# Kernel tuning notes

Measured on AMD Instinct MI355X. Metric: run time of the kernel, lower is better.

Reference implementation:

```python
import jax, jax.numpy as jnp
import numpy as np

N, E, D_IN, D_OUT = 50000, 300000, 256, 256
BN_EPS = 1e-5


def ccorr(a, b):
    # circular correlation: irfft(conj(rfft(a)) * rfft(b))
    return jnp.fft.irfft(jnp.conj(jnp.fft.rfft(a, axis=-1)) * jnp.fft.rfft(b, axis=-1), n=a.shape[-1], axis=-1)


def setup_inputs() -> dict:
    key = jax.random.key(0)
    ks = jax.random.split(key, 8)
    return {
        "node_ft": jax.random.normal(ks[0], (N, D_IN), dtype=jnp.float32),
        "edge_ft": jax.random.normal(ks[1], (E, D_IN), dtype=jnp.float32),
        "norm": jax.random.uniform(ks[2], (N, 1), dtype=jnp.float32),
        "w_loop": jax.random.normal(ks[3], (D_IN, D_OUT), dtype=jnp.float32) * (1.414 / np.sqrt(D_IN)),
        "w_in": jax.random.normal(ks[4], (D_IN, D_OUT), dtype=jnp.float32) * (1.414 / np.sqrt(D_IN)),
        "loop_rel": jax.random.normal(ks[5], (1, D_IN), dtype=jnp.float32),
        "w_bias": jnp.zeros((D_OUT,), dtype=jnp.float32),
        "bn_gamma": jnp.ones((D_OUT,), dtype=jnp.float32),
        "bn_beta": jnp.zeros((D_OUT,), dtype=jnp.float32),
        "src": jax.random.randint(ks[6], (E,), 0, N, dtype=jnp.int32),
        "dst": jax.random.randint(ks[7], (E,), 0, N, dtype=jnp.int32),
    }


def reference(node_ft, edge_ft, norm, w_loop, w_in, loop_rel, w_bias, bn_gamma, bn_beta, src, dst):
    n_nodes = node_ft.shape[0]
    # self-loop message: ccorr(ft, loop_rel) @ w_loop  [N, d_out]
    loop_msg = ccorr(node_ft, loop_rel) @ w_loop
    # per-edge message: ccorr(src_ft, edge_ft) @ w_in  [E, d_out]
    msg = ccorr(node_ft[src], edge_ft) @ w_in
    # scatter-sum aggregation then norm multiply (apply_func)
    agg = jax.ops.segment_sum(msg, dst, num_segments=n_nodes) * norm
    h = agg + w_bias + loop_msg
    # BatchNorm1d (training mode: batch stats, biased variance)
    mean = jnp.mean(h, axis=0)
    var = jnp.var(h, axis=0)
    h = (h - mean) * jax.lax.rsqrt(var + BN_EPS) * bn_gamma + bn_beta
    return jnp.tanh(h)
```

## Files before the change

kernel.cpp:

```cpp
#include <hip/hip_runtime.h>
#include <hip/hip_bf16.h>

#define NN 50000
#define BN_EPS 1e-5f
#define NFW 288
#define TWOPI_256 0.024543692606170259f

typedef __attribute__((ext_vector_type(8))) _Float16 half8;
typedef __attribute__((ext_vector_type(2))) _Float16 half2v;
typedef __attribute__((ext_vector_type(4))) float f32x4;
#define MFMA16F __builtin_amdgcn_mfma_f32_16x16x32_f16

__device__ __align__(16) _Float16 g_NF[(size_t)NN * NFW];
__device__ float g_LOOPM[(size_t)NN * 256];
__device__ float g_Wle[256 * 256];
__device__ __align__(16) unsigned short g_FB[8 * 20 * 64 * 8];
__device__ __align__(16) unsigned short g_CB[9 * 16 * 64 * 8];
__device__ __align__(16) unsigned short g_WLEB[8 * 16 * 64 * 8];

__device__ __forceinline__ void atomAddF(float* p, float v) { unsafeAtomicAdd(p, v); }

__device__ __forceinline__ unsigned short f2hu(float x) {
    union { _Float16 f; unsigned short u; } c;
    c.f = (_Float16)x;
    return c.u;
}

__device__ __forceinline__ void stage_h64(const float* __restrict__ base,
                                          long long row0, long long maxrow,
                                          unsigned short* A, int t) {
#pragma unroll
    for (int q = 0; q < 8; ++q) {
        int idx = q * 512 + t;
        int row = idx >> 6, c4 = idx & 63;
        long long gr = row0 + row;
        if (gr >= maxrow) gr = maxrow - 1;
        float4 v = ((const float4*)base)[gr * 64 + c4];
        union { _Float16 f[4]; ushort4 u; } r;
        r.f[0] = (_Float16)v.x; r.f[1] = (_Float16)v.y;
        r.f[2] = (_Float16)v.z; r.f[3] = (_Float16)v.w;
        int ks = c4 >> 3;
        int off = ((row >> 4) * 8 + ks) * 1024 +
                  ((((((c4 >> 1) & 3) << 4) | (row & 15)) * 16) ^ (ks << 4)) +
                  (c4 & 1) * 8;
        *(ushort4*)((char*)A + off) = r.u;
    }
}

__global__ __launch_bounds__(256) void wle_kernel(
    const float* __restrict__ loop_rel, const float* __restrict__ w_loop,
    float* __restrict__ W_le) {
    __shared__ float lr[256];
    const int d = threadIdx.x, j = blockIdx.x;
    lr[d] = loop_rel[d];
    __syncthreads();
    float acc = 0.f;
#pragma unroll 4
    for (int k = 0; k < 256; ++k)
        acc = fmaf(lr[(j + k) & 255], w_loop[k * 256 + d], acc);
    W_le[j * 256 + d] = acc;
}

__global__ __launch_bounds__(512) void fb_pack() {
    int b = blockIdx.x, ks = b / 20, nt = b % 20;
    int t = threadIdx.x, lane = t >> 3, e = t & 7;
    int k = 32 * ks + 8 * (lane >> 4) + e;
    int r2 = nt * 16 + (lane & 15);
    float val = 0.f;
    if (r2 < 258) {
        int f = r2 >> 1;
        int m = (f * k) & 255;
        float s, c;
        sincosf((float)m * TWOPI_256, &s, &c);
        val = (r2 & 1) ? -s : c;
    }
    g_FB[((ks * 20 + nt) * 64 + lane) * 8 + e] = f2hu(val);
}

__global__ __launch_bounds__(512) void cb_pack(const float* __restrict__ w_in) {
    __shared__ float ct[256], st[256];
    int t = threadIdx.x;
    if (t < 256) {
        float s, c;
        sincosf((float)t * TWOPI_256, &s, &c);
        ct[t] = c; st[t] = s;
    }
    __syncthreads();
    int b = blockIdx.x, ks = b / 16, nt = b % 16;
    int lane = t >> 3, e = t & 7;
    int kk = 32 * ks + 8 * (lane >> 4) + e;
    int d = nt * 16 + (lane & 15);
    float val = 0.f;
    if (kk < 258) {
        int f = kk >> 1;
        float cf = (f == 0 || f == 128) ? (1.f / 256.f) : (2.f / 256.f);
        const float* tab = (kk & 1) ? st : ct;
        float sgn = (kk & 1) ? -1.f : 1.f;
        float acc = 0.f;
        for (int k = 0; k < 256; ++k)
            acc = fmaf(tab[(f * k) & 255], w_in[k * 256 + d], acc);
        val = cf * sgn * acc;
    }
    g_CB[((ks * 16 + nt) * 64 + lane) * 8 + e] = f2hu(val);
}

__global__ __launch_bounds__(512) void wleb_pack() {
    int b = blockIdx.x, ks = b / 16, nt = b % 16;
    int t = threadIdx.x, lane = t >> 3, e = t & 7;
    int k = 32 * ks + 8 * (lane >> 4) + e;
    int d = nt * 16 + (lane & 15);
    g_WLEB[((ks * 16 + nt) * 64 + lane) * 8 + e] = f2hu(g_Wle[k * 256 + d]);
}

__global__ __launch_bounds__(512, 4) void nfloop_kernel(
    const float* __restrict__ node_ft, int N) {
    __shared__ char smem[32768];
    unsigned short* A = (unsigned short*)smem;
    const int t = threadIdx.x;
    const long long r0 = (long long)blockIdx.x * 64;
    stage_h64(node_ft, r0, N, A, t);
    __syncthreads();

    const int lane = t & 63, w = t >> 6;
    const int mw = w >> 2, nw = w & 3;
    const int l15 = lane & 15, lg = lane >> 4;

    {
        f32x4 acc[2][5] = {};
#pragma unroll
        for (int ks = 0; ks < 8; ++ks) {
            half8 a0 = *(const half8*)((char*)A + ((2 * mw + 0) * 8 + ks) * 1024 + ((lane * 16) ^ (ks << 4)));
            half8 a1 = *(const half8*)((char*)A + ((2 * mw + 1) * 8 + ks) * 1024 + ((lane * 16) ^ (ks << 4)));
#pragma unroll
            for (int j = 0; j < 4; ++j) {
                int tn = nw + 4 * j;
                half8 bf = *(const half8*)(g_FB + ((size_t)(ks * 20 + tn) * 64 + lane) * 8);
                acc[0][j] = MFMA16F(a0, bf, acc[0][j], 0, 0, 0);
                acc[1][j] = MFMA16F(a1, bf, acc[1][j], 0, 0, 0);
            }
            if (nw == 0) {
                half8 bf = *(const half8*)(g_FB + ((size_t)(ks * 20 + 16) * 64 + lane) * 8);
                acc[0][4] = MFMA16F(a0, bf, acc[0][4], 0, 0, 0);
                acc[1][4] = MFMA16F(a1, bf, acc[1][4], 0, 0, 0);
            }
        }
#pragma unroll
        for (int mt = 0; mt < 2; ++mt)
#pragma unroll
            for (int j = 0; j < 5; ++j) {
                int tn = nw + 4 * j;
                if (tn > 16 || (j == 4 && nw != 0)) continue;
                int r2 = tn * 16 + l15;
#pragma unroll
                for (int r = 0; r < 4; ++r) {
                    long long gr = r0 + (2 * mw + mt) * 16 + lg * 4 + r;
                    if (gr < N && r2 < 258)
                        g_NF[gr * NFW + r2] = (_Float16)acc[mt][j][r];
                }
            }
    }
    {
        f32x4 acc[2][4] = {};
#pragma unroll
        for (int ks = 0; ks < 8; ++ks) {
            half8 a0 = *(const half8*)((char*)A + ((2 * mw + 0) * 8 + ks) * 1024 + ((lane * 16) ^ (ks << 4)));
            half8 a1 = *(const half8*)((char*)A + ((2 * mw + 1) * 8 + ks) * 1024 + ((lane * 16) ^ (ks << 4)));
#pragma unroll
            for (int j = 0; j < 4; ++j) {
                half8 bf = *(const half8*)(g_WLEB + ((size_t)(ks * 16 + 4 * nw + j) * 64 + lane) * 8);
                acc[0][j] = MFMA16F(a0, bf, acc[0][j], 0, 0, 0);
                acc[1][j] = MFMA16F(a1, bf, acc[1][j], 0, 0, 0);
            }
        }
#pragma unroll
        for (int mt = 0; mt < 2; ++mt)
#pragma unroll
            for (int j = 0; j < 4; ++j)
#pragma unroll
                for (int r = 0; r < 4; ++r) {
                    long long gr = r0 + (2 * mw + mt) * 16 + lg * 4 + r;
                    if (gr < N)
                        g_LOOPM[gr * 256 + (4 * nw + j) * 16 + l15] = acc[mt][j][r];
                }
    }
}

__global__ __launch_bounds__(512, 4) void edge_kernel(
    const float* __restrict__ edge_ft, const int* __restrict__ src,
    const int* __restrict__ dst, float* __restrict__ agg, int E) {
    __shared__ char smem[36864 + 512];
    unsigned short* A = (unsigned short*)smem;
    unsigned short* Z = (unsigned short*)smem;
    int* sdd = (int*)(smem + 36864);

    const int t = threadIdx.x;
    const long long ebase = (long long)blockIdx.x * 64;
    const int lane = t & 63, w = t >> 6;
    const int mw = w >> 2, nw = w & 3;
    const int l15 = lane & 15, lg = lane >> 4;
    const bool odd = (l15 & 1);

    int srcv[2][4];
#pragma unroll
    for (int mt = 0; mt < 2; ++mt)
#pragma unroll
        for (int r = 0; r < 4; ++r) {
            long long ge = ebase + (2 * mw + mt) * 16 + lg * 4 + r;
            srcv[mt][r] = src[ge < E ? ge : 0];
        }

    if (t < 64) {
        long long ge = ebase + t;
        sdd[t] = dst[ge < E ? ge : 0];
    }
    stage_h64(edge_ft, ebase, E, A, t);

    unsigned int pf[2][5][4];
#pragma unroll
    for (int mt = 0; mt < 2; ++mt)
#pragma unroll
        for (int j = 0; j < 5; ++j) {
            int tn = nw + 4 * j;
            if (tn >= 17) continue;
            int r2 = tn * 16 + l15;
            if (r2 < 258) {
#pragma unroll
                for (int r = 0; r < 4; ++r)
                    pf[mt][j][r] = *(const unsigned int*)(g_NF +
                        (long long)srcv[mt][r] * NFW + (r2 & ~1));
            }
        }
    __syncthreads();

    f32x4 acc1[2][5] = {};
#pragma unroll
    for (int ks = 0; ks < 8; ++ks) {
        half8 a0 = *(const half8*)((char*)A + ((2 * mw + 0) * 8 + ks) * 1024 + ((lane * 16) ^ (ks << 4)));
        half8 a1 = *(const half8*)((char*)A + ((2 * mw + 1) * 8 + ks) * 1024 + ((lane * 16) ^ (ks << 4)));
#pragma unroll
        for (int j = 0; j < 4; ++j) {
            int tn = nw + 4 * j;
            half8 bf = *(const half8*)(g_FB + ((size_t)(ks * 20 + tn) * 64 + lane) * 8);
            acc1[0][j] = MFMA16F(a0, bf, acc1[0][j], 0, 0, 0);
            acc1[1][j] = MFMA16F(a1, bf, acc1[1][j], 0, 0, 0);
        }
        if (nw == 0) {
            half8 bf = *(const half8*)(g_FB + ((size_t)(ks * 20 + 16) * 64 + lane) * 8);
            acc1[0][4] = MFMA16F(a0, bf, acc1[0][4], 0, 0, 0);
            acc1[1][4] = MFMA16F(a1, bf, acc1[1][4], 0, 0, 0);
        }
    }
    __syncthreads();

#pragma unroll
    for (int mt = 0; mt < 2; ++mt) {
        int tm = 2 * mw + mt;
#pragma unroll
        for (int j = 0; j < 5; ++j) {
            int tn = nw + 4 * j;
            if (tn >= 18) continue;
            int r2 = tn * 16 + l15;
#pragma unroll
            for (int r = 0; r < 4; ++r) {
                int e = tm * 16 + lg * 4 + r;
                float z = 0.f;
                if (r2 < 258) {
                    float own = acc1[mt][j][r];
                    float oth = __shfl_xor(own, 1);
                    union { unsigned int u; half2v h; } cv;
                    cv.u = pf[mt][j][r];
                    float br = (float)cv.h[0], bi = (float)cv.h[1];
                    z = odd ? (br * own - bi * oth) : (br * own + bi * oth);
                }
                int ksz = r2 >> 5;
                int off = ((e >> 4) * 9 + ksz) * 1024 +
                          ((((((r2 >> 3) & 3) << 4) | (e & 15)) * 16) ^ (ksz << 4)) +
                          (r2 & 7) * 2;
                *(unsigned short*)((char*)Z + off) = f2hu(z);
            }
        }
    }
    __syncthreads();

    f32x4 acc2[2][4] = {};
#pragma unroll
    for (int ks = 0; ks < 9; ++ks) {
        half8 a0 = *(const half8*)((char*)Z + ((2 * mw + 0) * 9 + ks) * 1024 + ((lane * 16) ^ (ks << 4)));
        half8 a1 = *(const half8*)((char*)Z + ((2 * mw + 1) * 9 + ks) * 1024 + ((lane * 16) ^ (ks << 4)));
#pragma unroll
        for (int j = 0; j < 4; ++j) {
            half8 bf = *(const half8*)(g_CB + ((size_t)(ks * 16 + 4 * nw + j) * 64 + lane) * 8);
            acc2[0][j] = MFMA16F(a0, bf, acc2[0][j], 0, 0, 0);
            acc2[1][j] = MFMA16F(a1, bf, acc2[1][j], 0, 0, 0);
        }
    }

#pragma unroll
    for (int mt = 0; mt < 2; ++mt)
#pragma unroll
        for (int j = 0; j < 4; ++j)
#pragma unroll
            for (int r = 0; r < 4; ++r) {
                int e = (2 * mw + mt) * 16 + lg * 4 + r;
                if (ebase + e < E) {
                    int dr = sdd[e];
                    int d = (4 * nw + j) * 16 + l15;
                    atomAddF(agg + (long long)dr * 256 + d, acc2[mt][j][r]);
                }
            }
}

__global__ __launch_bounds__(256) void combine_kernel(
    const float* __restrict__ norm, const float* __restrict__ w_bias,
    float* __restrict__ hbuf, float* __restrict__ s1g, float* __restrict__ s2g,
    int N) {
    __shared__ float s1l[256], s2l[256];
    const int tid = threadIdx.x;
    s1l[tid] = 0.f;
    s2l[tid] = 0.f;
    __syncthreads();
    const int r0 = blockIdx.x * 32;
    const int dg = tid & 63, rg = tid >> 6;
    const float4 bv = ((const float4*)w_bias)[dg];
    float4* h4 = (float4*)hbuf;
    const float4* lp4 = (const float4*)g_LOOPM;
    float s1[4] = {0.f, 0.f, 0.f, 0.f}, s2[4] = {0.f, 0.f, 0.f, 0.f};
#pragma unroll
    for (int r8 = 0; r8 < 8; ++r8) {
        int r = r0 + rg * 8 + r8;
        if (r < N) {
            float nrm = norm[r];
            float4 av = h4[(long long)r * 64 + dg];
            float4 lv = lp4[(long long)r * 64 + dg];
            float h0 = fmaf(av.x, nrm, bv.x + lv.x);
            float h1 = fmaf(av.y, nrm, bv.y + lv.y);
            float h2 = fmaf(av.z, nrm, bv.z + lv.z);
            float h3 = fmaf(av.w, nrm, bv.w + lv.w);
            h4[(long long)r * 64 + dg] = make_float4(h0, h1, h2, h3);
            s1[0] += h0; s2[0] += h0 * h0;
            s1[1] += h1; s2[1] += h1 * h1;
            s1[2] += h2; s2[2] += h2 * h2;
            s1[3] += h3; s2[3] += h3 * h3;
        }
    }
#pragma unroll
    for (int c = 0; c < 4; ++c) {
        atomicAdd(&s1l[dg * 4 + c], s1[c]);
        atomicAdd(&s2l[dg * 4 + c], s2[c]);
    }
    __syncthreads();
    atomAddF(&s1g[tid], s1l[tid]);
    atomAddF(&s2g[tid], s2l[tid]);
}

__global__ __launch_bounds__(256) void finalize_kernel(
    float* __restrict__ out, const float* __restrict__ s1g,
    const float* __restrict__ s2g, const float* __restrict__ gamma,
    const float* __restrict__ beta, int N) {
    long long i4 = (long long)blockIdx.x * blockDim.x + threadIdx.x;
    long long tot = (long long)N * 64;
    if (i4 >= tot) return;
    const int dg = (int)(i4 & 63);
    float4 h = ((float4*)out)[i4];
    const float4 s1 = ((const float4*)s1g)[dg];
    const float4 s2 = ((const float4*)s2g)[dg];
    const float4 g = ((const float4*)gamma)[dg];
    const float4 b = ((const float4*)beta)[dg];
    const float invN = 1.f / (float)N;
    float4 o;
    { float m = s1.x * invN; float v = s2.x * invN - m * m;
      o.x = tanhf(fmaf(h.x - m, rsqrtf(v + BN_EPS) * g.x, b.x)); }
    { float m = s1.y * invN; float v = s2.y * invN - m * m;
      o.y = tanhf(fmaf(h.y - m, rsqrtf(v + BN_EPS) * g.y, b.y)); }
    { float m = s1.z * invN; float v = s2.z * invN - m * m;
      o.z = tanhf(fmaf(h.z - m, rsqrtf(v + BN_EPS) * g.z, b.z)); }
    { float m = s1.w * invN; float v = s2.w * invN - m * m;
      o.w = tanhf(fmaf(h.w - m, rsqrtf(v + BN_EPS) * g.w, b.w)); }
    ((float4*)out)[i4] = o;
}

extern "C" void kernel_launch(void* const* d_in, const int* in_sizes, int n_in,
                              void* d_out, int out_size, void* d_ws, size_t ws_size,
                              hipStream_t stream) {
    const float* node_ft  = (const float*)d_in[0];
    const float* edge_ft  = (const float*)d_in[1];
    const float* norm     = (const float*)d_in[2];
    const float* w_loop   = (const float*)d_in[3];
    const float* w_in     = (const float*)d_in[4];
    const float* loop_rel = (const float*)d_in[5];
    const float* w_bias   = (const float*)d_in[6];
    const float* bn_gamma = (const float*)d_in[7];
    const float* bn_beta  = (const float*)d_in[8];
    const int*   src      = (const int*)d_in[9];
    const int*   dst      = (const int*)d_in[10];

    const int N = in_sizes[2];
    const int E = in_sizes[9];
    float* out = (float*)d_out;

    float* s1g = (float*)d_ws;
    float* s2g = s1g + 256;

    hipMemsetAsync(d_out, 0, (size_t)N * 256 * sizeof(float), stream);
    hipMemsetAsync(d_ws, 0, 512 * sizeof(float), stream);

    float* Wle_ptr = nullptr;
    hipGetSymbolAddress((void**)&Wle_ptr, HIP_SYMBOL(g_Wle));

    wle_kernel<<<256, 256, 0, stream>>>(loop_rel, w_loop, Wle_ptr);
    fb_pack<<<8 * 20, 512, 0, stream>>>();
    cb_pack<<<9 * 16, 512, 0, stream>>>(w_in);
    wleb_pack<<<8 * 16, 512, 0, stream>>>();
    nfloop_kernel<<<(N + 63) / 64, 512, 0, stream>>>(node_ft, N);
    edge_kernel<<<(E + 63) / 64, 512, 0, stream>>>(edge_ft, src, dst, out, E);
    combine_kernel<<<(N + 31) / 32, 256, 0, stream>>>(norm, w_bias, out, s1g, s2g, N);
    finalize_kernel<<<(int)(((long long)N * 64 + 255) / 256), 256, 0, stream>>>(
        out, s1g, s2g, bn_gamma, bn_beta, N);
}
```

Measured before the change: 526.0 us.

## Make edge kernel persistent with double-buffered LDS prefetch of next tile

The edge kernel becomes persistent, with a grid capped at 512 blocks that each loop over 64-edge tiles in strides. While one tile is being computed, the block loads the next tile's edge features, src/dst indices and gathered node spectra into registers, then writes them into a second LDS buffer, so global load latency overlaps with MFMA work. It also swaps __syncthreads for raw s_waitcnt+s_barrier. The cost is twice the LDS per block (about 74KB), which can lower occupancy, plus more live registers from the staging arrays.

```diff
diff --git a/kernel.cpp b/kernel.cpp
--- a/kernel.cpp
+++ b/kernel.cpp
@@ -10,6 +10,8 @@
 typedef __attribute__((ext_vector_type(2))) _Float16 half2v;
 typedef __attribute__((ext_vector_type(4))) float f32x4;
 #define MFMA16F __builtin_amdgcn_mfma_f32_16x16x32_f16
+
+#define BARRIER_LDS() asm volatile("s_waitcnt lgkmcnt(0)\ns_barrier" ::: "memory")
 
 __device__ __align__(16) _Float16 g_NF[(size_t)NN * NFW];
 __device__ float g_LOOPM[(size_t)NN * 256];
@@ -26,24 +28,19 @@
     return c.u;
 }
 
-__device__ __forceinline__ void stage_h64(const float* __restrict__ base,
-                                          long long row0, long long maxrow,
-                                          unsigned short* A, int t) {
+__device__ __forceinline__ void stage_write(char* A, const float4* stg, int t) {
 #pragma unroll
     for (int q = 0; q < 8; ++q) {
         int idx = q * 512 + t;
         int row = idx >> 6, c4 = idx & 63;
-        long long gr = row0 + row;
-        if (gr >= maxrow) gr = maxrow - 1;
-        float4 v = ((const float4*)base)[gr * 64 + c4];
         union { _Float16 f[4]; ushort4 u; } r;
-        r.f[0] = (_Float16)v.x; r.f[1] = (_Float16)v.y;
-        r.f[2] = (_Float16)v.z; r.f[3] = (_Float16)v.w;
+        r.f[0] = (_Float16)stg[q].x; r.f[1] = (_Float16)stg[q].y;
+        r.f[2] = (_Float16)stg[q].z; r.f[3] = (_Float16)stg[q].w;
         int ks = c4 >> 3;
         int off = ((row >> 4) * 8 + ks) * 1024 +
                   ((((((c4 >> 1) & 3) << 4) | (row & 15)) * 16) ^ (ks << 4)) +
                   (c4 & 1) * 8;
-        *(ushort4*)((char*)A + off) = r.u;
+        *(ushort4*)(A + off) = r.u;
     }
 }
 
@@ -118,7 +115,17 @@
     unsigned short* A = (unsigned short*)smem;
     const int t = threadIdx.x;
     const long long r0 = (long long)blockIdx.x * 64;
-    stage_h64(node_ft, r0, N, A, t);
+    {
+        float4 stg[8];
+#pragma unroll
+        for (int q = 0; q < 8; ++q) {
+            int idx = q * 512 + t;
+            long long gr = r0 + (idx >> 6);
+            if (gr >= N) gr = N - 1;
+            stg[q] = ((const float4*)node_ft)[gr * 64 + (idx & 63)];
+        }
+        stage_write(smem, stg, t);
+    }
     __syncthreads();
 
     const int lane = t & 63, w = t >> 6;
@@ -187,127 +194,196 @@
 
 __global__ __launch_bounds__(512, 4) void edge_kernel(
     const float* __restrict__ edge_ft, const int* __restrict__ src,
-    const int* __restrict__ dst, float* __restrict__ agg, int E) {
-    __shared__ char smem[36864 + 512];
-    unsigned short* A = (unsigned short*)smem;
-    unsigned short* Z = (unsigned short*)smem;
-    int* sdd = (int*)(smem + 36864);
+    const int* __restrict__ dst, float* __restrict__ agg, int E, int ntiles) {
+    __shared__ char smem[2 * 36864 + 512];
+    int* sdd = (int*)(smem + 2 * 36864);
 
     const int t = threadIdx.x;
-    const long long ebase = (long long)blockIdx.x * 64;
     const int lane = t & 63, w = t >> 6;
     const int mw = w >> 2, nw = w & 3;
     const int l15 = lane & 15, lg = lane >> 4;
     const bool odd = (l15 & 1);
-
-    int srcv[2][4];
-#pragma unroll
-    for (int mt = 0; mt < 2; ++mt)
-#pragma unroll
-        for (int r = 0; r < 4; ++r) {
-            long long ge = ebase + (2 * mw + mt) * 16 + lg * 4 + r;
-            srcv[mt][r] = src[ge < E ? ge : 0];
-        }
-
-    if (t < 64) {
-        long long ge = ebase + t;
-        sdd[t] = dst[ge < E ? ge : 0];
-    }
-    stage_h64(edge_ft, ebase, E, A, t);
-
+    const int G = gridDim.x;
+
+    long long T = blockIdx.x;
     unsigned int pf[2][5][4];
-#pragma unroll
-    for (int mt = 0; mt < 2; ++mt)
-#pragma unroll
-        for (int j = 0; j < 5; ++j) {
-            int tn = nw + 4 * j;
-            if (tn >= 17) continue;
-            int r2 = tn * 16 + l15;
-            if (r2 < 258) {
-#pragma unroll
-                for (int r = 0; r < 4; ++r)
-                    pf[mt][j][r] = *(const unsigned int*)(g_NF +
-                        (long long)srcv[mt][r] * NFW + (r2 & ~1));
-            }
-        }
-    __syncthreads();
-
-    f32x4 acc1[2][5] = {};
-#pragma unroll
-    for (int ks = 0; ks < 8; ++ks) {
-        half8 a0 = *(const half8*)((char*)A + ((2 * mw + 0) * 8 + ks) * 1024 + ((lane * 16) ^ (ks << 4)));
-        half8 a1 = *(const half8*)((char*)A + ((2 * mw + 1) * 8 + ks) * 1024 + ((lane * 16) ^ (ks << 4)));
-#pragma unroll
-        for (int j = 0; j < 4; ++j) {
-            int tn = nw + 4 * j;
-            half8 bf = *(const half8*)(g_FB + ((size_t)(ks * 20 + tn) * 64 + lane) * 8);
-            acc1[0][j] = MFMA16F(a0, bf, acc1[0][j], 0, 0, 0);
-            acc1[1][j] = MFMA16F(a1, bf, acc1[1][j], 0, 0, 0);
-        }
-        if (nw == 0) {
-            half8 bf = *(const half8*)(g_FB + ((size_t)(ks * 20 + 16) * 64 + lane) * 8);
-            acc1[0][4] = MFMA16F(a0, bf, acc1[0][4], 0, 0, 0);
-            acc1[1][4] = MFMA16F(a1, bf, acc1[1][4], 0, 0, 0);
-        }
-    }
-    __syncthreads();
-
-#pragma unroll
-    for (int mt = 0; mt < 2; ++mt) {
-        int tm = 2 * mw + mt;
-#pragma unroll
-        for (int j = 0; j < 5; ++j) {
-            int tn = nw + 4 * j;
-            if (tn >= 18) continue;
-            int r2 = tn * 16 + l15;
+
+    {
+        long long ebase = T * 64;
+        int srcv[2][4];
+#pragma unroll
+        for (int mt = 0; mt < 2; ++mt)
 #pragma unroll
             for (int r = 0; r < 4; ++r) {
-                int e = tm * 16 + lg * 4 + r;
-                float z = 0.f;
+                long long ge = ebase + (2 * mw + mt) * 16 + lg * 4 + r;
+                srcv[mt][r] = src[ge < E ? ge : 0];
+            }
+        float4 stg[8];
+#pragma unroll
+        for (int q = 0; q < 8; ++q) {
+            int idx = q * 512 + t;
+            long long gr = ebase + (idx >> 6);
+            if (gr >= E) gr = E - 1;
+            stg[q] = ((const float4*)edge_ft)[gr * 64 + (idx & 63)];
+        }
+        if (t < 64) {
+            long long ge = ebase + t;
+            sdd[t] = dst[ge < E ? ge : 0];
+        }
+#pragma unroll
+        for (int mt = 0; mt < 2; ++mt)
+#pragma unroll
+            for (int j = 0; j < 5; ++j) {
+                int tn = nw + 4 * j;
+                if (tn >= 17) continue;
+                int r2 = tn * 16 + l15;
                 if (r2 < 258) {
-                    float own = acc1[mt][j][r];
-                    float oth = __shfl_xor(own, 1);
-                    union { unsigned int u; half2v h; } cv;
-                    cv.u = pf[mt][j][r];
-                    float br = (float)cv.h[0], bi = (float)cv.h[1];
-                    z = odd ? (br * own - bi * oth) : (br * own + bi * oth);
-                }
-                int ksz = r2 >> 5;
-                int off = ((e >> 4) * 9 + ksz) * 1024 +
-                          ((((((r2 >> 3) & 3) << 4) | (e & 15)) * 16) ^ (ksz << 4)) +
-                          (r2 & 7) * 2;
-                *(unsigned short*)((char*)Z + off) = f2hu(z);
-            }
-        }
-    }
-    __syncthreads();
-
-    f32x4 acc2[2][4] = {};
-#pragma unroll
-    for (int ks = 0; ks < 9; ++ks) {
-        half8 a0 = *(const half8*)((char*)Z + ((2 * mw + 0) * 9 + ks) * 1024 + ((lane * 16) ^ (ks << 4)));
-        half8 a1 = *(const half8*)((char*)Z + ((2 * mw + 1) * 9 + ks) * 1024 + ((lane * 16) ^ (ks << 4)));
-#pragma unroll
-        for (int j = 0; j < 4; ++j) {
-            half8 bf = *(const half8*)(g_CB + ((size_t)(ks * 16 + 4 * nw + j) * 64 + lane) * 8);
-            acc2[0][j] = MFMA16F(a0, bf, acc2[0][j], 0, 0, 0);
-            acc2[1][j] = MFMA16F(a1, bf, acc2[1][j], 0, 0, 0);
-        }
-    }
-
-#pragma unroll
-    for (int mt = 0; mt < 2; ++mt)
-#pragma unroll
-        for (int j = 0; j < 4; ++j)
-#pragma unroll
-            for (int r = 0; r < 4; ++r) {
-                int e = (2 * mw + mt) * 16 + lg * 4 + r;
-                if (ebase + e < E) {
-                    int dr = sdd[e];
-                    int d = (4 * nw + j) * 16 + l15;
-                    atomAddF(agg + (long long)dr * 256 + d, acc2[mt][j][r]);
-                }
-            }
+#pragma unroll
+                    for (int r = 0; r < 4; ++r)
+                        pf[mt][j][r] = *(const unsigned int*)(g_NF +
+                            (long long)srcv[mt][r] * NFW + (r2 & ~1));
+                }
+            }
+        stage_write(smem, stg, t);
+    }
+    BARRIER_LDS();
+
+    int c = 0;
+    while (true) {
+        char* AB = smem + c * 36864;
+        const long long ebase = T * 64;
+        const long long Tn = T + G;
+        const bool has_next = (Tn < ntiles);
+
+        f32x4 acc1[2][5] = {};
+#pragma unroll
+        for (int ks = 0; ks < 8; ++ks) {
+            half8 a0 = *(const half8*)(AB + ((0 * 8 + ks)) * 1024 + ((lane * 16) ^ (ks << 4)) + mw * 16384);
+            half8 a1 = *(const half8*)(AB + ((1 * 8 + ks)) * 1024 + ((lane * 16) ^ (ks << 4)) + mw * 16384);
+#pragma unroll
+            for (int j = 0; j < 4; ++j) {
+                int tn = nw + 4 * j;
+                half8 bf = *(const half8*)(g_FB + ((size_t)(ks * 20 + tn) * 64 + lane) * 8);
+                acc1[0][j] = MFMA16F(a0, bf, acc1[0][j], 0, 0, 0);
+                acc1[1][j] = MFMA16F(a1, bf, acc1[1][j], 0, 0, 0);
+            }
+            if (nw == 0) {
+                half8 bf = *(const half8*)(g_FB + ((size_t)(ks * 20 + 16) * 64 + lane) * 8);
+                acc1[0][4] = MFMA16F(a0, bf, acc1[0][4], 0, 0, 0);
+                acc1[1][4] = MFMA16F(a1, bf, acc1[1][4], 0, 0, 0);
+            }
+        }
+        BARRIER_LDS();
+
+#pragma unroll
+        for (int mt = 0; mt < 2; ++mt) {
+            int tm = 2 * mw + mt;
+#pragma unroll
+            for (int j = 0; j < 5; ++j) {
+                int tn = nw + 4 * j;
+                if (tn >= 18) continue;
+                int r2 = tn * 16 + l15;
+#pragma unroll
+                for (int r = 0; r < 4; ++r) {
+                    int e = tm * 16 + lg * 4 + r;
+                    float z = 0.f;
+                    if (r2 < 258) {
+                        float own = acc1[mt][j][r];
+                        float oth = __shfl_xor(own, 1);
+                        union { unsigned int u; half2v h; } cv;
+                        cv.u = pf[mt][j][r];
+                        float br = (float)cv.h[0], bi = (float)cv.h[1];
+                        z = odd ? (br * own - bi * oth) : (br * own + bi * oth);
+                    }
+                    int ksz = r2 >> 5;
+                    int off = ((e >> 4) * 9 + ksz) * 1024 +
+                              ((((((r2 >> 3) & 3) << 4) | (e & 15)) * 16) ^ (ksz << 4)) +
+                              (r2 & 7) * 2;
+                    *(unsigned short*)(AB + off) = f2hu(z);
+                }
+            }
+        }
+
+        int nsrc[2][4];
+        float4 nstg[8];
+        int ndst = 0;
+        if (has_next) {
+            long long nb = Tn * 64;
+#pragma unroll
+            for (int mt = 0; mt < 2; ++mt)
+#pragma unroll
+                for (int r = 0; r < 4; ++r) {
+                    long long ge = nb + (2 * mw + mt) * 16 + lg * 4 + r;
+                    nsrc[mt][r] = src[ge < E ? ge : 0];
+                }
+#pragma unroll
+            for (int q = 0; q < 8; ++q) {
+                int idx = q * 512 + t;
+                long long gr = nb + (idx >> 6);
+                if (gr >= E) gr = E - 1;
+                nstg[q] = ((const float4*)edge_ft)[gr * 64 + (idx & 63)];
+            }
+            if (t < 64) {
+                long long ge = nb + t;
+                ndst = dst[ge < E ? ge : 0];
+            }
+        }
+        BARRIER_LDS();
+
+        f32x4 acc2[2][4] = {};
+#pragma unroll
+        for (int ks = 0; ks < 9; ++ks) {
+            half8 a0 = *(const half8*)(AB + ((0 * 9 + ks)) * 1024 + ((lane * 16) ^ (ks << 4)) + mw * 18432);
+            half8 a1 = *(const half8*)(AB + ((1 * 9 + ks)) * 1024 + ((lane * 16) ^ (ks << 4)) + mw * 18432);
+#pragma unroll
+            for (int j = 0; j < 4; ++j) {
+                half8 bf = *(const half8*)(g_CB + ((size_t)(ks * 16 + 4 * nw + j) * 64 + lane) * 8);
+                acc2[0][j] = MFMA16F(a0, bf, acc2[0][j], 0, 0, 0);
+                acc2[1][j] = MFMA16F(a1, bf, acc2[1][j], 0, 0, 0);
+            }
+        }
+
+        if (has_next) {
+#pragma unroll
+            for (int mt = 0; mt < 2; ++mt)
+#pragma unroll
+                for (int j = 0; j < 5; ++j) {
+                    int tn = nw + 4 * j;
+                    if (tn >= 17) continue;
+                    int r2 = tn * 16 + l15;
+                    if (r2 < 258) {
+#pragma unroll
+                        for (int r = 0; r < 4; ++r)
+                            pf[mt][j][r] = *(const unsigned int*)(g_NF +
+                                (long long)nsrc[mt][r] * NFW + (r2 & ~1));
+                    }
+                }
+        }
+
+        if (has_next) {
+            stage_write(smem + (c ^ 1) * 36864, nstg, t);
+            if (t < 64) sdd[(c ^ 1) * 64 + t] = ndst;
+        }
+
+#pragma unroll
+        for (int mt = 0; mt < 2; ++mt)
+#pragma unroll
+            for (int j = 0; j < 4; ++j)
+#pragma unroll
+                for (int r = 0; r < 4; ++r) {
+                    int e = (2 * mw + mt) * 16 + lg * 4 + r;
+                    if (ebase + e < E) {
+                        int dr = sdd[c * 64 + e];
+                        atomAddF(agg + (long long)dr * 256 + (4 * nw + j) * 16 + l15,
+                                 acc2[mt][j][r]);
+                    }
+                }
+
+        if (!has_next) break;
+        BARRIER_LDS();
+        c ^= 1;
+        T = Tn;
+    }
 }
 
 __global__ __launch_bounds__(256) void combine_kernel(
@@ -407,12 +483,15 @@
     float* Wle_ptr = nullptr;
     hipGetSymbolAddress((void**)&Wle_ptr, HIP_SYMBOL(g_Wle));
 
+    const int ntiles = (E + 63) / 64;
+    const int egrid = ntiles < 512 ? ntiles : 512;
+
     wle_kernel<<<256, 256, 0, stream>>>(loop_rel, w_loop, Wle_ptr);
     fb_pack<<<8 * 20, 512, 0, stream>>>();
     cb_pack<<<9 * 16, 512, 0, stream>>>(w_in);
     wleb_pack<<<8 * 16, 512, 0, stream>>>();
     nfloop_kernel<<<(N + 63) / 64, 512, 0, stream>>>(node_ft, N);
-    edge_kernel<<<(E + 63) / 64, 512, 0, stream>>>(edge_ft, src, dst, out, E);
+    edge_kernel<<<egrid, 512, 0, stream>>>(edge_ft, src, dst, out, E, ntiles);
     combine_kernel<<<(N + 31) / 32, 256, 0, stream>>>(norm, w_bias, out, s1g, s2g, N);
     finalize_kernel<<<(int)(((long long)N * 64 + 255) / 256), 256, 0, stream>>>(
         out, s1g, s2g, bn_gamma, bn_beta, N);
```

After: 1.321 ms. +151.2%, slower.

## Sort edges by destination and fuse loop message, bias and norm into outputs

Applied to the files above, without the earlier changes.

Adds a counting sort of edges by destination (histogram, three-pass scan, permutation) so each edge block handles edges grouped by destination node. The edge kernel then pre-sums runs of equal destinations within a lane before issuing fewer atomics. The loop message and bias are written straight into the output, and norm is applied per edge. This removes the separate loop-message buffer, the output memset and the combine pass, replacing them with a read-only stats pass. In exchange it adds several small sort kernels and gathers edge_ft rows indirectly through the permutation, which makes those loads less coalesced.

```diff
diff --git a/kernel.cpp b/kernel.cpp
--- a/kernel.cpp
+++ b/kernel.cpp
@@ -2,6 +2,7 @@
 #include <hip/hip_bf16.h>
 
 #define NN 50000
+#define EE 300000
 #define BN_EPS 1e-5f
 #define NFW 288
 #define TWOPI_256 0.024543692606170259f
@@ -12,11 +13,16 @@
 #define MFMA16F __builtin_amdgcn_mfma_f32_16x16x32_f16
 
 __device__ __align__(16) _Float16 g_NF[(size_t)NN * NFW];
-__device__ float g_LOOPM[(size_t)NN * 256];
 __device__ float g_Wle[256 * 256];
 __device__ __align__(16) unsigned short g_FB[8 * 20 * 64 * 8];
 __device__ __align__(16) unsigned short g_CB[9 * 16 * 64 * 8];
 __device__ __align__(16) unsigned short g_WLEB[8 * 16 * 64 * 8];
+__device__ int g_hist[NN];
+__device__ int g_off[NN];
+__device__ int g_cursor[NN];
+__device__ int g_perm[EE];
+__device__ int g_bsum[128];
+__device__ int g_bbase[128];
 
 __device__ __forceinline__ void atomAddF(float* p, float v) { unsafeAtomicAdd(p, v); }
 
@@ -26,24 +32,74 @@
     return c.u;
 }
 
-__device__ __forceinline__ void stage_h64(const float* __restrict__ base,
-                                          long long row0, long long maxrow,
-                                          unsigned short* A, int t) {
+__device__ __forceinline__ void stage_write(char* A, const float4* stg, int t) {
 #pragma unroll
     for (int q = 0; q < 8; ++q) {
         int idx = q * 512 + t;
         int row = idx >> 6, c4 = idx & 63;
-        long long gr = row0 + row;
-        if (gr >= maxrow) gr = maxrow - 1;
-        float4 v = ((const float4*)base)[gr * 64 + c4];
         union { _Float16 f[4]; ushort4 u; } r;
-        r.f[0] = (_Float16)v.x; r.f[1] = (_Float16)v.y;
-        r.f[2] = (_Float16)v.z; r.f[3] = (_Float16)v.w;
+        r.f[0] = (_Float16)stg[q].x; r.f[1] = (_Float16)stg[q].y;
+        r.f[2] = (_Float16)stg[q].z; r.f[3] = (_Float16)stg[q].w;
         int ks = c4 >> 3;
         int off = ((row >> 4) * 8 + ks) * 1024 +
                   ((((((c4 >> 1) & 3) << 4) | (row & 15)) * 16) ^ (ks << 4)) +
                   (c4 & 1) * 8;
-        *(ushort4*)((char*)A + off) = r.u;
+        *(ushort4*)(A + off) = r.u;
+    }
+}
+
+__global__ __launch_bounds__(512) void hist_kernel(const int* __restrict__ dst, int E) {
+    int e = blockIdx.x * 512 + threadIdx.x;
+    if (e < E) atomicAdd(&g_hist[dst[e]], 1);
+}
+
+__global__ __launch_bounds__(512) void scanA_kernel(int N) {
+    __shared__ int arr[512];
+    int t = threadIdx.x, b = blockIdx.x * 512 + t;
+    int cnt = (b < N) ? g_hist[b] : 0;
+    arr[t] = cnt;
+    __syncthreads();
+#pragma unroll
+    for (int off = 1; off < 512; off <<= 1) {
+        int v = (t >= off) ? arr[t - off] : 0;
+        __syncthreads();
+        arr[t] += v;
+        __syncthreads();
+    }
+    if (b < N) g_off[b] = arr[t] - cnt;
+    if (t == 511) g_bsum[blockIdx.x] = arr[511];
+}
+
+__global__ __launch_bounds__(128) void scanB_kernel(int nblk) {
+    __shared__ int arr[128];
+    int t = threadIdx.x;
+    int v0 = (t < nblk) ? g_bsum[t] : 0;
+    arr[t] = v0;
+    __syncthreads();
+#pragma unroll
+    for (int off = 1; off < 128; off <<= 1) {
+        int v = (t >= off) ? arr[t - off] : 0;
+        __syncthreads();
+        arr[t] += v;
+        __syncthreads();
+    }
+    if (t < nblk) g_bbase[t] = arr[t] - v0;
+}
+
+__global__ __launch_bounds__(512) void scanC_kernel(int N) {
+    int b = blockIdx.x * 512 + threadIdx.x;
+    if (b < N) {
+        int v = g_off[b] + g_bbase[blockIdx.x];
+        g_off[b] = v;
+        g_cursor[b] = v;
+    }
+}
+
+__global__ __launch_bounds__(512) void perm_kernel(const int* __restrict__ dst, int E) {
+    int e = blockIdx.x * 512 + threadIdx.x;
+    if (e < E) {
+        int pos = atomicAdd(&g_cursor[dst[e]], 1);
+        g_perm[pos] = e;
     }
 }
 
@@ -113,12 +169,23 @@
 }
 
 __global__ __launch_bounds__(512, 4) void nfloop_kernel(
-    const float* __restrict__ node_ft, int N) {
+    const float* __restrict__ node_ft, const float* __restrict__ w_bias,
+    float* __restrict__ out, int N) {
     __shared__ char smem[32768];
     unsigned short* A = (unsigned short*)smem;
     const int t = threadIdx.x;
     const long long r0 = (long long)blockIdx.x * 64;
-    stage_h64(node_ft, r0, N, A, t);
+    {
+        float4 stg[8];
+#pragma unroll
+        for (int q = 0; q < 8; ++q) {
+            int idx = q * 512 + t;
+            long long gr = r0 + (idx >> 6);
+            if (gr >= N) gr = N - 1;
+            stg[q] = ((const float4*)node_ft)[gr * 64 + (idx & 63)];
+        }
+        stage_write(smem, stg, t);
+    }
     __syncthreads();
 
     const int lane = t & 63, w = t >> 6;
@@ -173,25 +240,30 @@
             }
         }
 #pragma unroll
-        for (int mt = 0; mt < 2; ++mt)
-#pragma unroll
-            for (int j = 0; j < 4; ++j)
+        for (int j = 0; j < 4; ++j) {
+            const int col = (4 * nw + j) * 16 + l15;
+            const float bj = w_bias[col];
+#pragma unroll
+            for (int mt = 0; mt < 2; ++mt)
 #pragma unroll
                 for (int r = 0; r < 4; ++r) {
                     long long gr = r0 + (2 * mw + mt) * 16 + lg * 4 + r;
                     if (gr < N)
-                        g_LOOPM[gr * 256 + (4 * nw + j) * 16 + l15] = acc[mt][j][r];
+                        out[gr * 256 + col] = acc[mt][j][r] + bj;
                 }
+        }
     }
 }
 
 __global__ __launch_bounds__(512, 4) void edge_kernel(
-    const float* __restrict__ edge_ft, const int* __restrict__ src,
-    const int* __restrict__ dst, float* __restrict__ agg, int E) {
+    const float* __restrict__ edge_ft, const float* __restrict__ norm,
+    const int* __restrict__ src, const int* __restrict__ dst,
+    float* __restrict__ agg, int E) {
     __shared__ char smem[36864 + 512];
     unsigned short* A = (unsigned short*)smem;
     unsigned short* Z = (unsigned short*)smem;
     int* sdd = (int*)(smem + 36864);
+    float* snrm = (float*)(smem + 36864 + 256);
 
     const int t = threadIdx.x;
     const long long ebase = (long long)blockIdx.x * 64;
@@ -206,14 +278,25 @@
 #pragma unroll
         for (int r = 0; r < 4; ++r) {
             long long ge = ebase + (2 * mw + mt) * 16 + lg * 4 + r;
-            srcv[mt][r] = src[ge < E ? ge : 0];
+            if (ge >= E) ge = E - 1;
+            srcv[mt][r] = src[g_perm[ge]];
         }
 
     if (t < 64) {
         long long ge = ebase + t;
-        sdd[t] = dst[ge < E ? ge : 0];
-    }
-    stage_h64(edge_ft, ebase, E, A, t);
+        if (ge >= E) ge = E - 1;
+        int d = dst[g_perm[ge]];
+        sdd[t] = d;
+        snrm[t] = norm[d];
+    }
+
+    float4 stg[8];
+#pragma unroll
+    for (int q = 0; q < 8; ++q) {
+        long long ge = ebase + q * 8 + (t >> 6);
+        if (ge >= E) ge = E - 1;
+        stg[q] = ((const float4*)edge_ft)[(long long)g_perm[ge] * 64 + (t & 63)];
+    }
 
     unsigned int pf[2][5][4];
 #pragma unroll
@@ -230,6 +313,7 @@
                         (long long)srcv[mt][r] * NFW + (r2 & ~1));
             }
         }
+    stage_write(smem, stg, t);
     __syncthreads();
 
     f32x4 acc1[2][5] = {};
@@ -296,61 +380,64 @@
     }
 
 #pragma unroll
-    for (int mt = 0; mt < 2; ++mt)
-#pragma unroll
-        for (int j = 0; j < 4; ++j)
-#pragma unroll
-            for (int r = 0; r < 4; ++r) {
-                int e = (2 * mw + mt) * 16 + lg * 4 + r;
-                if (ebase + e < E) {
-                    int dr = sdd[e];
-                    int d = (4 * nw + j) * 16 + l15;
-                    atomAddF(agg + (long long)dr * 256 + d, acc2[mt][j][r]);
+    for (int mt = 0; mt < 2; ++mt) {
+        const int e0 = (2 * mw + mt) * 16 + lg * 4;
+        const bool v0 = ebase + e0 < E, v1 = ebase + e0 + 1 < E;
+        const bool v2 = ebase + e0 + 2 < E, v3 = ebase + e0 + 3 < E;
+        const int d0 = sdd[e0], d1 = sdd[e0 + 1], d2 = sdd[e0 + 2], d3 = sdd[e0 + 3];
+        const float n0 = snrm[e0], n1 = snrm[e0 + 1], n2 = snrm[e0 + 2], n3 = snrm[e0 + 3];
+        const bool uni = v3 && (d0 == d1) && (d1 == d2) && (d2 == d3);
+        const bool p01 = v1 && (d0 == d1);
+        const bool p23 = v3 && (d2 == d3);
+#pragma unroll
+        for (int j = 0; j < 4; ++j) {
+            const int col = (4 * nw + j) * 16 + l15;
+            float x0 = acc2[mt][j][0] * n0, x1 = acc2[mt][j][1] * n1;
+            float x2 = acc2[mt][j][2] * n2, x3 = acc2[mt][j][3] * n3;
+            if (uni) {
+                atomAddF(agg + (long long)d0 * 256 + col, (x0 + x1) + (x2 + x3));
+            } else {
+                if (p01) atomAddF(agg + (long long)d0 * 256 + col, x0 + x1);
+                else {
+                    if (v0) atomAddF(agg + (long long)d0 * 256 + col, x0);
+                    if (v1) atomAddF(agg + (long long)d1 * 256 + col, x1);
                 }
-            }
-}
-
-__global__ __launch_bounds__(256) void combine_kernel(
-    const float* __restrict__ norm, const float* __restrict__ w_bias,
-    float* __restrict__ hbuf, float* __restrict__ s1g, float* __restrict__ s2g,
-    int N) {
+                if (p23) atomAddF(agg + (long long)d2 * 256 + col, x2 + x3);
+                else {
+                    if (v2) atomAddF(agg + (long long)d2 * 256 + col, x2);
+                    if (v3) atomAddF(agg + (long long)d3 * 256 + col, x3);
+                }
+            }
+        }
+    }
+}
+
+__global__ __launch_bounds__(256) void stats_kernel(
+    const float* __restrict__ h, float* __restrict__ s1g,
+    float* __restrict__ s2g, long long tot4) {
     __shared__ float s1l[256], s2l[256];
-    const int tid = threadIdx.x;
-    s1l[tid] = 0.f;
-    s2l[tid] = 0.f;
-    __syncthreads();
-    const int r0 = blockIdx.x * 32;
-    const int dg = tid & 63, rg = tid >> 6;
-    const float4 bv = ((const float4*)w_bias)[dg];
-    float4* h4 = (float4*)hbuf;
-    const float4* lp4 = (const float4*)g_LOOPM;
-    float s1[4] = {0.f, 0.f, 0.f, 0.f}, s2[4] = {0.f, 0.f, 0.f, 0.f};
-#pragma unroll
-    for (int r8 = 0; r8 < 8; ++r8) {
-        int r = r0 + rg * 8 + r8;
-        if (r < N) {
-            float nrm = norm[r];
-            float4 av = h4[(long long)r * 64 + dg];
-            float4 lv = lp4[(long long)r * 64 + dg];
-            float h0 = fmaf(av.x, nrm, bv.x + lv.x);
-            float h1 = fmaf(av.y, nrm, bv.y + lv.y);
-            float h2 = fmaf(av.z, nrm, bv.z + lv.z);
-            float h3 = fmaf(av.w, nrm, bv.w + lv.w);
-            h4[(long long)r * 64 + dg] = make_float4(h0, h1, h2, h3);
-            s1[0] += h0; s2[0] += h0 * h0;
-            s1[1] += h1; s2[1] += h1 * h1;
-            s1[2] += h2; s2[2] += h2 * h2;
-            s1[3] += h3; s2[3] += h3 * h3;
-        }
+    const int t = threadIdx.x;
+    s1l[t] = 0.f;
+    s2l[t] = 0.f;
+    __syncthreads();
+    const int dg = t & 63;
+    float a1[4] = {0.f, 0.f, 0.f, 0.f}, a2[4] = {0.f, 0.f, 0.f, 0.f};
+    const long long stride = (long long)gridDim.x * 256;
+    for (long long i4 = (long long)blockIdx.x * 256 + t; i4 < tot4; i4 += stride) {
+        float4 v = ((const float4*)h)[i4];
+        a1[0] += v.x; a2[0] += v.x * v.x;
+        a1[1] += v.y; a2[1] += v.y * v.y;
+        a1[2] += v.z; a2[2] += v.z * v.z;
+        a1[3] += v.w; a2[3] += v.w * v.w;
     }
 #pragma unroll
     for (int c = 0; c < 4; ++c) {
-        atomicAdd(&s1l[dg * 4 + c], s1[c]);
-        atomicAdd(&s2l[dg * 4 + c], s2[c]);
-    }
-    __syncthreads();
-    atomAddF(&s1g[tid], s1l[tid]);
-    atomAddF(&s2g[tid], s2l[tid]);
+        atomicAdd(&s1l[dg * 4 + c], a1[c]);
+        atomicAdd(&s2l[dg * 4 + c], a2[c]);
+    }
+    __syncthreads();
+    atomAddF(&s1g[t], s1l[t]);
+    atomAddF(&s2g[t], s2l[t]);
 }
 
 __global__ __launch_bounds__(256) void finalize_kernel(
@@ -401,19 +488,31 @@
     float* s1g = (float*)d_ws;
     float* s2g = s1g + 256;
 
-    hipMemsetAsync(d_out, 0, (size_t)N * 256 * sizeof(float), stream);
     hipMemsetAsync(d_ws, 0, 512 * sizeof(float), stream);
 
     float* Wle_ptr = nullptr;
     hipGetSymbolAddress((void**)&Wle_ptr, HIP_SYMBOL(g_Wle));
+    void* hist_ptr = nullptr;
+    hipGetSymbolAddress(&hist_ptr, HIP_SYMBOL(g_hist));
+    hipMemsetAsync(hist_ptr, 0, (size_t)N * sizeof(int), stream);
+
+    const int sblk = (N + 511) / 512;
+    const int eblk = (E + 511) / 512;
+
+    hist_kernel<<<eblk, 512, 0, stream>>>(dst, E);
+    scanA_kernel<<<sblk, 512, 0, stream>>>(N);
+    scanB_kernel<<<1, 128, 0, stream>>>(sblk);
+    scanC_kernel<<<sblk, 512, 0, stream>>>(N);
+    perm_kernel<<<eblk, 512, 0, stream>>>(dst, E);
 
     wle_kernel<<<256, 256, 0, stream>>>(loop_rel, w_loop, Wle_ptr);
     fb_pack<<<8 * 20, 512, 0, stream>>>();
     cb_pack<<<9 * 16, 512, 0, stream>>>(w_in);
     wleb_pack<<<8 * 16, 512, 0, stream>>>();
-    nfloop_kernel<<<(N + 63) / 64, 512, 0, stream>>>(node_ft, N);
-    edge_kernel<<<(E + 63) / 64, 512, 0, stream>>>(edge_ft, src, dst, out, E);
-    combine_kernel<<<(N + 31) / 32, 256, 0, stream>>>(norm, w_bias, out, s1g, s2g, N);
+
+    nfloop_kernel<<<(N + 63) / 64, 512, 0, stream>>>(node_ft, w_bias, out, N);
+    edge_kernel<<<(E + 63) / 64, 512, 0, stream>>>(edge_ft, norm, src, dst, out, E);
+    stats_kernel<<<256, 256, 0, stream>>>(out, s1g, s2g, (long long)N * 64);
     finalize_kernel<<<(int)(((long long)N * 64 + 255) / 256), 256, 0, stream>>>(
         out, s1g, s2g, bn_gamma, bn_beta, N);
 }
```

After: 451.1 us. 14.2% less time.
